# Kernel optimization log

Measured on AMD Instinct MI355X. Metric: run time of the kernel, lower is better.

The kernel has to match this reference:

```python
import jax, jax.numpy as jnp
import numpy as np

B, H, W, C = 64, 224, 224, 3
P = 16
DIM = 768
DEPTH = 12
NH, DH = 12, 64
FF = 3072
NPATCH = (H // P) * (W // P)   # 196
L = NPATCH + 1                 # 197 tokens (CLS + patches)
KEEP = int(L * (1.0 - 0.75))   # 49 unmasked tokens


def setup_inputs() -> dict:
    key = jax.random.key(0)
    ks = jax.random.split(key, 16)
    s = 0.02
    inp = {
        'inputs': jax.random.normal(ks[0], (B, H, W, C), jnp.float32),
        'conv_w': jax.random.normal(ks[1], (P, P, C, DIM), jnp.float32) * s,
        'ct':     jax.random.normal(ks[2], (1, 1, DIM), jnp.float32) * s,
        'pe':     jax.random.normal(ks[3], (1, L, DIM), jnp.float32) * s,
        'ln1_s': jnp.ones((DEPTH, DIM), jnp.float32),
        'ln1_b': jnp.zeros((DEPTH, DIM), jnp.float32),
        'qkv_w': jax.random.normal(ks[4], (DEPTH, DIM, 3 * NH * DH), jnp.float32) * s,
        'proj_w': jax.random.normal(ks[5], (DEPTH, NH * DH, DIM), jnp.float32) * s,
        'ln2_s': jnp.ones((DEPTH, DIM), jnp.float32),
        'ln2_b': jnp.zeros((DEPTH, DIM), jnp.float32),
        'w1': jax.random.normal(ks[6], (DEPTH, DIM, FF), jnp.float32) * s,
        'b1': jnp.zeros((DEPTH, FF), jnp.float32),
        'w2': jax.random.normal(ks[7], (DEPTH, FF, DIM), jnp.float32) * s,
        'b2': jnp.zeros((DEPTH, DIM), jnp.float32),
        # Faithful to original: permutation of arange(1, L+1); max value 197
        # is out-of-range and gets clamped by JAX gather, exactly as upstream.
        'mask_idx': jax.random.permutation(ks[8], jnp.arange(1, L + 1))[:KEEP].astype(jnp.int32),
    }
    return inp


def _layernorm(x, scale, bias, eps=1e-9):
    m = jnp.mean(x, axis=-1, keepdims=True)
    v = jnp.var(x, axis=-1, keepdims=True)
    return (x - m) * jax.lax.rsqrt(v + eps) * scale + bias


def _encoder(x, layer_params):
    # x: [B, KEEP, DIM]; layer_params leaves stacked on axis 0 (DEPTH)
    inv_sqrt_d = 1.0 / jnp.sqrt(jnp.float32(DH))

    def block(x, p):
        ln1s, ln1b, qw, pw, ln2s, ln2b, w1, b1, w2, b2 = p
        h = _layernorm(x, ln1s, ln1b)
        qkv = h @ qw                                   # [B, Lk, 3*NH*DH]
        q, k, v = jnp.split(qkv, 3, axis=-1)
        def heads(t):
            return t.reshape(x.shape[0], -1, NH, DH).transpose(0, 2, 1, 3)
        q, k, v = heads(q), heads(k), heads(v)         # [B, NH, Lk, DH]
        att = jax.nn.softmax(jnp.einsum('bhqd,bhkd->bhqk', q, k) * inv_sqrt_d)
        o = jnp.einsum('bhqk,bhkd->bhqd', att, v)
        o = o.transpose(0, 2, 1, 3).reshape(x.shape[0], -1, NH * DH) @ pw
        x = x + o
        h2 = _layernorm(x, ln2s, ln2b)
        x = x + (jax.nn.gelu(h2 @ w1 + b1) @ w2 + b2)
        return x, None

    x, _ = jax.lax.scan(block, x, layer_params)
    return x


def reference(inputs, conv_w, ct, pe, ln1_s, ln1_b, qkv_w, proj_w,
              ln2_s, ln2_b, w1, b1, w2, b2, mask_idx):
    # patch embed: stride-P conv, no bias
    out = jax.lax.conv_general_dilated(
        inputs, conv_w, window_strides=(P, P), padding='VALID',
        dimension_numbers=('NHWC', 'HWIO', 'NHWC'))      # [B, 14, 14, DIM]
    out = out.reshape(out.shape[0], -1, out.shape[3])     # [B, 196, DIM]
    out = jnp.concatenate((jnp.repeat(ct, out.shape[0], axis=0), out), axis=1)
    out = out + pe                                        # [B, 197, DIM]
    patches = out[:, mask_idx]                            # [B, 49, DIM]
    layer_params = (ln1_s, ln1_b, qkv_w, proj_w, ln2_s, ln2_b, w1, b1, w2, b2)
    return _encoder(patches, layer_params)
```

## Files before the change

kernel.cpp:

```cpp
#include <hip/hip_runtime.h>
#include <hip/hip_bf16.h>
#include <math.h>

#define DIMV   768
#define BATCH  64
#define KEEPT  49
#define MTOK   (BATCH*KEEPT)
#define NHEADS 12
#define DHEAD  64
#define FFV    3072
#define NDEPTH 12

typedef short short8 __attribute__((ext_vector_type(8)));
typedef float floatx4 __attribute__((ext_vector_type(4)));
typedef unsigned short ushort;
typedef unsigned short ushortx8 __attribute__((ext_vector_type(8)));

__device__ __forceinline__ ushort f2bf(float f) {
  __hip_bfloat16 h = __float2bfloat16(f);
  return *(ushort*)&h;
}

__device__ __forceinline__ void async_cp16(const void* g, void* l) {
  __builtin_amdgcn_global_load_lds((const __attribute__((address_space(1))) void*)g,
                                   (__attribute__((address_space(3))) void*)l,
                                   16, 0, 0);
}

__global__ __launch_bounds__(256) void gather_patches(
    const float* __restrict__ inp, const int* __restrict__ mask,
    __hip_bfloat16* __restrict__ apix)
{
  int gid = blockIdx.x * 256 + threadIdx.x;
  if (gid >= MTOK * DIMV) return;
  int r = gid / DIMV, k = gid - r * DIMV;
  int b = r / KEEPT, t = r - b * KEEPT;
  int j = mask[t];
  j = j < 0 ? 0 : (j > 196 ? 196 : j);
  float v = 0.f;
  if (j > 0) {
    int p  = j - 1, py = p / 14, px = p - py * 14;
    int ky = k / 48, rem = k - ky * 48, kx = rem / 3, c = rem - kx * 3;
    v = inp[(((b * 224) + py * 16 + ky) * 224 + px * 16 + kx) * 3 + c];
  }
  apix[gid] = __float2bfloat16(v);
}

__global__ __launch_bounds__(256) void layernorm_k(
    const float* __restrict__ x, const float* __restrict__ sc,
    const float* __restrict__ bi, __hip_bfloat16* __restrict__ out)
{
  __shared__ float red[8];
  int r = blockIdx.x;
  const float* xr = x + (size_t)r * DIMV;
  int t = threadIdx.x;
  float v[3];
  float s = 0.f, ss = 0.f;
#pragma unroll
  for (int i = 0; i < 3; i++) {
    float a = xr[t + i * 256];
    v[i] = a; s += a; ss += a * a;
  }
#pragma unroll
  for (int off = 32; off > 0; off >>= 1) {
    s  += __shfl_down(s,  off, 64);
    ss += __shfl_down(ss, off, 64);
  }
  int wave = t >> 6, lane = t & 63;
  if (lane == 0) { red[wave] = s; red[4 + wave] = ss; }
  __syncthreads();
  if (t == 0) {
    float a  = red[0] + red[1] + red[2] + red[3];
    float b2 = red[4] + red[5] + red[6] + red[7];
    float m  = a * (1.f / DIMV);
    float var = b2 * (1.f / DIMV) - m * m;
    red[0] = m;
    red[1] = rsqrtf(var + 1e-9f);
  }
  __syncthreads();
  float m = red[0], rs = red[1];
  __hip_bfloat16* outr = out + (size_t)r * DIMV;
#pragma unroll
  for (int i = 0; i < 3; i++) {
    int d = t + i * 256;
    outr[d] = __float2bfloat16((v[i] - m) * rs * sc[d] + bi[d]);
  }
}

__device__ __forceinline__ void transpose_tile64(
    const float* __restrict__ src, __hip_bfloat16* __restrict__ dst,
    int R, int C, int tr, int tcc)
{
  __shared__ float lds[64][65];
  const int tid = threadIdx.x;
  const int r0 = tr * 64, c0 = tcc * 64;
  const int lr = tid >> 4, lc4 = (tid & 15) * 4;
#pragma unroll
  for (int p = 0; p < 4; p++) {
    float4 v = *(const float4*)(src + (size_t)(r0 + p * 16 + lr) * C + c0 + lc4);
    lds[p * 16 + lr][lc4 + 0] = v.x;
    lds[p * 16 + lr][lc4 + 1] = v.y;
    lds[p * 16 + lr][lc4 + 2] = v.z;
    lds[p * 16 + lr][lc4 + 3] = v.w;
  }
  __syncthreads();
  const int c = tid >> 2, rc = (tid & 3) * 8;
  ushortx8 o0, o1;
#pragma unroll
  for (int j = 0; j < 8; j++) o0[j] = f2bf(lds[rc + j][c]);
#pragma unroll
  for (int j = 0; j < 8; j++) o1[j] = f2bf(lds[rc + 32 + j][c]);
  ushort* drow = (ushort*)dst + (size_t)(c0 + c) * R + r0;
  *(ushortx8*)(drow + rc)      = o0;
  *(ushortx8*)(drow + rc + 32) = o1;
}

__global__ __launch_bounds__(256) void transpose_one(
    const float* __restrict__ src, __hip_bfloat16* __restrict__ dst, int R, int C)
{
  int tc = C >> 6;
  transpose_tile64(src, dst, R, C, blockIdx.x / tc, blockIdx.x % tc);
}

#define QKV_TE  ((size_t)2304*768)
#define PROJ_TE ((size_t)768*768)
#define W1_TE   ((size_t)3072*768)
#define W2_TE   ((size_t)768*3072)
#define LSTRIDE (QKV_TE + PROJ_TE + W1_TE + W2_TE)

__global__ __launch_bounds__(256) void convert_weights(
    const float* __restrict__ qkv_w, const float* __restrict__ proj_w,
    const float* __restrict__ w1, const float* __restrict__ w2,
    __hip_bfloat16* __restrict__ dstBase, int layer0, size_t dstStride)
{
  int l = layer0 + blockIdx.y;
  __hip_bfloat16* d = dstBase + (size_t)blockIdx.y * dstStride;
  int tile = blockIdx.x;
  const float* src; __hip_bfloat16* dst; int R, C, t0;
  if (tile < 432)       { src = qkv_w  + (size_t)l*768*2304; dst = d;                          R=768;  C=2304; t0=tile; }
  else if (tile < 576)  { src = proj_w + (size_t)l*768*768;  dst = d + QKV_TE;                 R=768;  C=768;  t0=tile-432; }
  else if (tile < 1152) { src = w1     + (size_t)l*768*3072; dst = d + QKV_TE+PROJ_TE;         R=768;  C=3072; t0=tile-576; }
  else                  { src = w2     + (size_t)l*3072*768; dst = d + QKV_TE+PROJ_TE+W1_TE;   R=3072; C=768;  t0=tile-1152; }
  int tc = C >> 6;
  transpose_tile64(src, dst, R, C, t0 / tc, t0 % tc);
}

enum { EPI_NONE = 0, EPI_RESID = 1, EPI_BIAS_GELU = 2, EPI_BIAS_RESID = 3,
       EPI_EMBED = 4 };

template <int TN, int EPI, bool OUT_BF16>
__global__ __launch_bounds__(256) void gemm_mfma(
    const ushort* __restrict__ A, const ushort* __restrict__ Bt,
    const float* __restrict__ Cin, const float* __restrict__ bias,
    const float* __restrict__ pe, const int* __restrict__ mask,
    void* __restrict__ Cout, int M, int N, int K)
{
  constexpr int AM = (TN == 128) ? 4 : 2;
  constexpr int B_LOADS = TN / 64;
  __shared__ ushort As[128 * 32];
  __shared__ ushort Bs[TN * 32];

  const int tid  = threadIdx.x;
  const int wave = tid >> 6, lane = tid & 63;
  const int bm = blockIdx.y, bn = blockIdx.x;

  const int wm0 = (TN == 128) ? (wave & 1) * 64 : wave * 32;
  const int wn0 = (TN == 128) ? (wave >> 1) * 64 : 0;

  floatx4 acc[AM][4];
#pragma unroll
  for (int i = 0; i < AM; i++)
#pragma unroll
    for (int j = 0; j < 4; j++) { floatx4 z = {0.f,0.f,0.f,0.f}; acc[i][j] = z; }

  const int lrow = lane >> 2, lchunk = (lane & 3) * 8;
  const ushort* aSrc[2];
  ushort*       aDst[2];
#pragma unroll
  for (int i = 0; i < 2; i++) {
    int row = bm * 128 + (wave * 2 + i) * 16 + lrow;
    row = row < M - 1 ? row : M - 1;
    aSrc[i] = A + (size_t)row * K + lchunk;
    aDst[i] = As + (wave * 2 + i) * 512;
  }
  const ushort* bSrc[B_LOADS];
  ushort*       bDst[B_LOADS];
#pragma unroll
  for (int i = 0; i < B_LOADS; i++) {
    int row = bn * TN + (wave * B_LOADS + i) * 16 + lrow;
    bSrc[i] = Bt + (size_t)row * K + lchunk;
    bDst[i] = Bs + (wave * B_LOADS + i) * 512;
  }

  for (int k0 = 0; k0 < K; k0 += 32) {
    __syncthreads();
#pragma unroll
    for (int i = 0; i < 2; i++)       async_cp16(aSrc[i] + k0, aDst[i]);
#pragma unroll
    for (int i = 0; i < B_LOADS; i++) async_cp16(bSrc[i] + k0, bDst[i]);
    __syncthreads();

    short8 af[AM], bf[4];
#pragma unroll
    for (int mt = 0; mt < AM; mt++)
      af[mt] = *(const short8*)&As[(wm0 + mt * 16 + (lane & 15)) * 32 + (lane >> 4) * 8];
#pragma unroll
    for (int nt = 0; nt < 4; nt++)
      bf[nt] = *(const short8*)&Bs[(wn0 + nt * 16 + (lane & 15)) * 32 + (lane >> 4) * 8];
#pragma unroll
    for (int mt = 0; mt < AM; mt++)
#pragma unroll
      for (int nt = 0; nt < 4; nt++)
        acc[mt][nt] = __builtin_amdgcn_mfma_f32_16x16x32_bf16(af[mt], bf[nt], acc[mt][nt], 0, 0, 0);
  }

  const int colb = bn * TN + wn0 + (lane & 15);
  const int rq   = (lane >> 4) * 4;
#pragma unroll
  for (int mt = 0; mt < AM; mt++) {
#pragma unroll
    for (int r = 0; r < 4; r++) {
      int row = bm * 128 + wm0 + mt * 16 + rq + r;
      if (row >= M) continue;
#pragma unroll
      for (int nt = 0; nt < 4; nt++) {
        int col = colb + nt * 16;
        float u = acc[mt][nt][r];
        if (EPI == EPI_BIAS_GELU || EPI == EPI_BIAS_RESID) u += bias[col];
        if (EPI == EPI_BIAS_GELU) {
          float t3 = u * u * u;
          u = 0.5f * u * (1.f + tanhf(0.7978845608028654f * (u + 0.044715f * t3)));
        }
        if (EPI == EPI_RESID || EPI == EPI_BIAS_RESID) u += Cin[(size_t)row * N + col];
        if (EPI == EPI_EMBED) {
          int t = row % KEEPT;
          int j = mask[t];
          j = j < 0 ? 0 : (j > 196 ? 196 : j);
          if (j == 0) u = bias[col];
          u += pe[(size_t)j * DIMV + col];
        }
        if (OUT_BF16)
          ((__hip_bfloat16*)Cout)[(size_t)row * N + col] = __float2bfloat16(u);
        else
          ((float*)Cout)[(size_t)row * N + col] = u;
      }
    }
  }
}

__global__ __launch_bounds__(256) void attn_mfma(
    const ushort* __restrict__ qkv, ushort* __restrict__ o)
{
  __shared__ ushort qA[64 * 72];
  __shared__ ushort kB[64 * 72];
  __shared__ ushort vT[64 * 72];
  __shared__ ushort pA[64 * 72];
  const int b = blockIdx.x, hh = blockIdx.y;
  const int tid = threadIdx.x;
  const int wave = tid >> 6, lane = tid & 63;
  const int fr = lane & 15, fc = lane >> 4;

  const ushort* base = qkv + (size_t)b * KEEPT * (3 * DIMV) + hh * 64;

#pragma unroll
  for (int it = 0; it < 2; it++) {
    int r  = it * 32 + wave * 8 + (lane >> 3);
    int cc = (lane & 7) * 8;
    short8 qv = {0,0,0,0,0,0,0,0};
    short8 kv = {0,0,0,0,0,0,0,0};
    if (r < KEEPT) {
      const ushort* row = base + (size_t)r * (3 * DIMV);
      qv = *(const short8*)(row + cc);
      kv = *(const short8*)(row + DIMV + cc);
    }
    *(short8*)&qA[r * 72 + cc] = qv;
    *(short8*)&kB[r * 72 + cc] = kv;
  }
  for (int r = wave; r < 64; r += 4) {
    ushort v = 0;
    if (r < KEEPT) v = base[(size_t)r * (3 * DIMV) + 2 * DIMV + lane];
    vT[lane * 72 + r] = v;
  }
  __syncthreads();

  const int q0 = wave * 16;
  floatx4 sacc[4];
#pragma unroll
  for (int nt = 0; nt < 4; nt++) { floatx4 z = {0.f,0.f,0.f,0.f}; sacc[nt] = z; }

#pragma unroll
  for (int kk = 0; kk < 2; kk++) {
    const int ch = kk * 32 + fc * 8;
    short8 af = *(const short8*)&qA[(q0 + fr) * 72 + ch];
#pragma unroll
    for (int nt = 0; nt < 4; nt++) {
      short8 bf = *(const short8*)&kB[(nt * 16 + fr) * 72 + ch];
      sacc[nt] = __builtin_amdgcn_mfma_f32_16x16x32_bf16(af, bf, sacc[nt], 0, 0, 0);
    }
  }

  float inv[4];
#pragma unroll
  for (int r = 0; r < 4; r++) {
    float mx = -1e30f;
#pragma unroll
    for (int nt = 0; nt < 4; nt++) {
      float s = sacc[nt][r] * 0.125f;
      if (nt == 3 && fr >= 1) s = -1e30f;
      sacc[nt][r] = s;
      mx = fmaxf(mx, s);
    }
    mx = fmaxf(mx, __shfl_xor(mx, 1, 64));
    mx = fmaxf(mx, __shfl_xor(mx, 2, 64));
    mx = fmaxf(mx, __shfl_xor(mx, 4, 64));
    mx = fmaxf(mx, __shfl_xor(mx, 8, 64));
    float sum = 0.f;
#pragma unroll
    for (int nt = 0; nt < 4; nt++) {
      float e = __expf(sacc[nt][r] - mx);
      sacc[nt][r] = e;
      sum += e;
    }
    sum += __shfl_xor(sum, 1, 64);
    sum += __shfl_xor(sum, 2, 64);
    sum += __shfl_xor(sum, 4, 64);
    sum += __shfl_xor(sum, 8, 64);
    inv[r] = 1.f / sum;
  }

#pragma unroll
  for (int r = 0; r < 4; r++)
#pragma unroll
    for (int nt = 0; nt < 4; nt++)
      pA[(q0 + fc * 4 + r) * 72 + nt * 16 + fr] = f2bf(sacc[nt][r]);
  __syncthreads();

  floatx4 oacc[4];
#pragma unroll
  for (int nt = 0; nt < 4; nt++) { floatx4 z = {0.f,0.f,0.f,0.f}; oacc[nt] = z; }

#pragma unroll
  for (int kk = 0; kk < 2; kk++) {
    const int ch = kk * 32 + fc * 8;
    short8 af = *(const short8*)&pA[(q0 + fr) * 72 + ch];
#pragma unroll
    for (int nt = 0; nt < 4; nt++) {
      short8 bf = *(const short8*)&vT[(nt * 16 + fr) * 72 + ch];
      oacc[nt] = __builtin_amdgcn_mfma_f32_16x16x32_bf16(af, bf, oacc[nt], 0, 0, 0);
    }
  }

  ushort* obase = o + (size_t)b * KEEPT * DIMV + hh * 64;
#pragma unroll
  for (int r = 0; r < 4; r++) {
    int q = q0 + fc * 4 + r;
    if (q < KEEPT) {
#pragma unroll
      for (int nt = 0; nt < 4; nt++)
        obase[(size_t)q * DIMV + nt * 16 + fr] = f2bf(oacc[nt][r] * inv[r]);
    }
  }
}

extern "C" void kernel_launch(void* const* d_in, const int* in_sizes, int n_in,
                              void* d_out, int out_size, void* d_ws, size_t ws_size,
                              hipStream_t stream)
{
  (void)in_sizes; (void)n_in; (void)out_size;
  const float* inputs = (const float*)d_in[0];
  const float* conv_w = (const float*)d_in[1];
  const float* ct     = (const float*)d_in[2];
  const float* pe     = (const float*)d_in[3];
  const float* ln1_s  = (const float*)d_in[4];
  const float* ln1_b  = (const float*)d_in[5];
  const float* qkv_w  = (const float*)d_in[6];
  const float* proj_w = (const float*)d_in[7];
  const float* ln2_s  = (const float*)d_in[8];
  const float* ln2_b  = (const float*)d_in[9];
  const float* w1     = (const float*)d_in[10];
  const float* b1     = (const float*)d_in[11];
  const float* w2     = (const float*)d_in[12];
  const float* b2     = (const float*)d_in[13];
  const int*   mask   = (const int*)d_in[14];
  float* out = (float*)d_out;

  char* wsb = (char*)d_ws;
  float*          x     = (float*)wsb;
  __hip_bfloat16* h     = (__hip_bfloat16*)(wsb + 9633792);
  __hip_bfloat16* big   = (__hip_bfloat16*)(wsb + 9633792 + 4816896);
  __hip_bfloat16* convT = (__hip_bfloat16*)(wsb + 9633792 + 4816896 + 19267584);
  __hip_bfloat16* wbuf  = (__hip_bfloat16*)(wsb + 9633792 + 4816896 + 19267584 + 1179648);
  const size_t base_bytes = 9633792ull + 4816896 + 19267584 + 1179648;
  const bool all_mode = ws_size >= base_bytes + 12ull * LSTRIDE * 2;

  __hip_bfloat16* apix = h;
  __hip_bfloat16* qkv  = big;
  __hip_bfloat16* g    = big;

  dim3 blk(256);
  const int nelem = MTOK * DIMV;
  const int nblk  = (nelem + 255) / 256;
  const int mg    = (MTOK + 127) / 128;

  transpose_one<<<144, blk, 0, stream>>>(conv_w, convT, 768, 768);
  if (all_mode)
    convert_weights<<<dim3(1728, 12), blk, 0, stream>>>(
        qkv_w, proj_w, w1, w2, wbuf, 0, LSTRIDE);

  gather_patches<<<nblk, blk, 0, stream>>>(inputs, mask, apix);
  gemm_mfma<64, EPI_EMBED, false><<<dim3(12, mg), blk, 0, stream>>>(
      (const ushort*)apix, (const ushort*)convT, nullptr, ct, pe, mask, x,
      MTOK, DIMV, DIMV);

  for (int l = 0; l < NDEPTH; l++) {
    __hip_bfloat16* wl = wbuf + (all_mode ? (size_t)l * LSTRIDE : 0);
    if (!all_mode)
      convert_weights<<<dim3(1728, 1), blk, 0, stream>>>(
          qkv_w, proj_w, w1, w2, wbuf, l, 0);
    const ushort* qkvT  = (const ushort*)wl;
    const ushort* projT = (const ushort*)(wl + QKV_TE);
    const ushort* w1T   = (const ushort*)(wl + QKV_TE + PROJ_TE);
    const ushort* w2T   = (const ushort*)(wl + QKV_TE + PROJ_TE + W1_TE);

    layernorm_k<<<MTOK, blk, 0, stream>>>(x, ln1_s + l * DIMV, ln1_b + l * DIMV, h);
    gemm_mfma<128, EPI_NONE, true><<<dim3(18, mg), blk, 0, stream>>>(
        (const ushort*)h, qkvT, nullptr, nullptr, nullptr, nullptr, qkv,
        MTOK, 3 * DIMV, DIMV);
    attn_mfma<<<dim3(BATCH, NHEADS), blk, 0, stream>>>(
        (const ushort*)qkv, (ushort*)h);
    gemm_mfma<64, EPI_RESID, false><<<dim3(12, mg), blk, 0, stream>>>(
        (const ushort*)h, projT, x, nullptr, nullptr, nullptr, x,
        MTOK, DIMV, DIMV);
    layernorm_k<<<MTOK, blk, 0, stream>>>(x, ln2_s + l * DIMV, ln2_b + l * DIMV, h);
    gemm_mfma<128, EPI_BIAS_GELU, true><<<dim3(24, mg), blk, 0, stream>>>(
        (const ushort*)h, w1T, nullptr, b1 + (size_t)l * FFV, nullptr, nullptr, g,
        MTOK, FFV, DIMV);
    float* dst = (l == NDEPTH - 1) ? out : x;
    gemm_mfma<64, EPI_BIAS_RESID, false><<<dim3(12, mg), blk, 0, stream>>>(
        (const ushort*)g, w2T, x, b2 + (size_t)l * DIMV, nullptr, nullptr, dst,
        MTOK, DIMV, FFV);
  }
}
```

Measured before the change: 2.495 ms.

## Double-buffer GEMM LDS tiles with BK=64, XOR swizzle, and unified 128x64 tiling

The MFMA GEMM now uses double-buffered LDS tiles with a K-step of 64. The next tile's async global-to-LDS copy is issued before the current tile's MFMAs, so there is one barrier per iteration instead of two. LDS columns are XOR-swizzled to reduce bank conflicts, and MFMA sections get raised wave priority. All GEMMs now use a single 128x64 tile shape, which doubles the grid for the QKV and FC1 GEMMs and raises LDS use per block, possibly lowering occupancy.

```diff
diff --git a/kernel.cpp b/kernel.cpp
--- a/kernel.cpp
+++ b/kernel.cpp
@@ -148,79 +148,109 @@
 enum { EPI_NONE = 0, EPI_RESID = 1, EPI_BIAS_GELU = 2, EPI_BIAS_RESID = 3,
        EPI_EMBED = 4 };
 
-template <int TN, int EPI, bool OUT_BF16>
+template <int EPI, bool OUT_BF16>
 __global__ __launch_bounds__(256) void gemm_mfma(
     const ushort* __restrict__ A, const ushort* __restrict__ Bt,
     const float* __restrict__ Cin, const float* __restrict__ bias,
     const float* __restrict__ pe, const int* __restrict__ mask,
     void* __restrict__ Cout, int M, int N, int K)
 {
-  constexpr int AM = (TN == 128) ? 4 : 2;
-  constexpr int B_LOADS = TN / 64;
-  __shared__ ushort As[128 * 32];
-  __shared__ ushort Bs[TN * 32];
+  __shared__ ushort As[2][128 * 64];
+  __shared__ ushort Bs[2][64 * 64];
 
   const int tid  = threadIdx.x;
   const int wave = tid >> 6, lane = tid & 63;
   const int bm = blockIdx.y, bn = blockIdx.x;
-
-  const int wm0 = (TN == 128) ? (wave & 1) * 64 : wave * 32;
-  const int wn0 = (TN == 128) ? (wave >> 1) * 64 : 0;
-
-  floatx4 acc[AM][4];
-#pragma unroll
-  for (int i = 0; i < AM; i++)
+  const int fr = lane & 15, fc = lane >> 4;
+
+  floatx4 acc[2][4];
+#pragma unroll
+  for (int i = 0; i < 2; i++)
 #pragma unroll
     for (int j = 0; j < 4; j++) { floatx4 z = {0.f,0.f,0.f,0.f}; acc[i][j] = z; }
 
-  const int lrow = lane >> 2, lchunk = (lane & 3) * 8;
-  const ushort* aSrc[2];
-  ushort*       aDst[2];
-#pragma unroll
-  for (int i = 0; i < 2; i++) {
-    int row = bm * 128 + (wave * 2 + i) * 16 + lrow;
+  const int lrow   = lane >> 3;
+  const int lchunk = ((lane & 7) ^ lrow) * 8;
+  const ushort* aSrc[4];
+#pragma unroll
+  for (int i = 0; i < 4; i++) {
+    int row = bm * 128 + wave * 32 + i * 8 + lrow;
     row = row < M - 1 ? row : M - 1;
     aSrc[i] = A + (size_t)row * K + lchunk;
-    aDst[i] = As + (wave * 2 + i) * 512;
-  }
-  const ushort* bSrc[B_LOADS];
-  ushort*       bDst[B_LOADS];
-#pragma unroll
-  for (int i = 0; i < B_LOADS; i++) {
-    int row = bn * TN + (wave * B_LOADS + i) * 16 + lrow;
+  }
+  const ushort* bSrc[2];
+#pragma unroll
+  for (int i = 0; i < 2; i++) {
+    int row = bn * 64 + wave * 16 + i * 8 + lrow;
     bSrc[i] = Bt + (size_t)row * K + lchunk;
-    bDst[i] = Bs + (wave * B_LOADS + i) * 512;
-  }
-
-  for (int k0 = 0; k0 < K; k0 += 32) {
-    __syncthreads();
-#pragma unroll
-    for (int i = 0; i < 2; i++)       async_cp16(aSrc[i] + k0, aDst[i]);
-#pragma unroll
-    for (int i = 0; i < B_LOADS; i++) async_cp16(bSrc[i] + k0, bDst[i]);
-    __syncthreads();
-
-    short8 af[AM], bf[4];
-#pragma unroll
-    for (int mt = 0; mt < AM; mt++)
-      af[mt] = *(const short8*)&As[(wm0 + mt * 16 + (lane & 15)) * 32 + (lane >> 4) * 8];
-#pragma unroll
-    for (int nt = 0; nt < 4; nt++)
-      bf[nt] = *(const short8*)&Bs[(wn0 + nt * 16 + (lane & 15)) * 32 + (lane >> 4) * 8];
-#pragma unroll
-    for (int mt = 0; mt < AM; mt++)
+  }
+
+  const int NT = K >> 6;
+
+  {
+    ushort* aD = &As[0][(wave * 32) * 64];
+#pragma unroll
+    for (int i = 0; i < 4; i++) async_cp16(aSrc[i], aD + i * 8 * 64);
+    ushort* bD = &Bs[0][(wave * 16) * 64];
+#pragma unroll
+    for (int i = 0; i < 2; i++) async_cp16(bSrc[i], bD + i * 8 * 64);
+  }
+  asm volatile("s_waitcnt vmcnt(0)" ::: "memory");
+  __builtin_amdgcn_s_barrier();
+  __builtin_amdgcn_sched_barrier(0);
+
+  int cur = 0;
+  for (int t = 0; t < NT; t++) {
+    if (t + 1 < NT) {
+      const int k0 = (t + 1) << 6;
+      ushort* aD = &As[cur ^ 1][(wave * 32) * 64];
+#pragma unroll
+      for (int i = 0; i < 4; i++) async_cp16(aSrc[i] + k0, aD + i * 8 * 64);
+      ushort* bD = &Bs[cur ^ 1][(wave * 16) * 64];
+#pragma unroll
+      for (int i = 0; i < 2; i++) async_cp16(bSrc[i] + k0, bD + i * 8 * 64);
+    }
+
+    const ushort* Ab = As[cur];
+    const ushort* Bb = Bs[cur];
+    short8 af[2][2], bf[2][4];
+#pragma unroll
+    for (int kk = 0; kk < 2; kk++) {
+      const int cbase = kk * 4 + fc;
+      const int slot  = (cbase ^ (fr & 7)) * 8;
+#pragma unroll
+      for (int mt = 0; mt < 2; mt++)
+        af[kk][mt] = *(const short8*)&Ab[(wave * 32 + mt * 16 + fr) * 64 + slot];
 #pragma unroll
       for (int nt = 0; nt < 4; nt++)
-        acc[mt][nt] = __builtin_amdgcn_mfma_f32_16x16x32_bf16(af[mt], bf[nt], acc[mt][nt], 0, 0, 0);
-  }
-
-  const int colb = bn * TN + wn0 + (lane & 15);
-  const int rq   = (lane >> 4) * 4;
-#pragma unroll
-  for (int mt = 0; mt < AM; mt++) {
+        bf[kk][nt] = *(const short8*)&Bb[(nt * 16 + fr) * 64 + slot];
+    }
+    __builtin_amdgcn_s_setprio(1);
+#pragma unroll
+    for (int kk = 0; kk < 2; kk++)
+#pragma unroll
+      for (int mt = 0; mt < 2; mt++)
+#pragma unroll
+        for (int nt = 0; nt < 4; nt++)
+          acc[mt][nt] = __builtin_amdgcn_mfma_f32_16x16x32_bf16(
+              af[kk][mt], bf[kk][nt], acc[mt][nt], 0, 0, 0);
+    __builtin_amdgcn_s_setprio(0);
+
+    if (t + 1 < NT) {
+      asm volatile("s_waitcnt vmcnt(0)" ::: "memory");
+      __builtin_amdgcn_s_barrier();
+      __builtin_amdgcn_sched_barrier(0);
+    }
+    cur ^= 1;
+  }
+
+  const int colb = bn * 64 + fr;
+  const int rq   = fc * 4;
+#pragma unroll
+  for (int mt = 0; mt < 2; mt++) {
 #pragma unroll
     for (int r = 0; r < 4; r++) {
-      int row = bm * 128 + wm0 + mt * 16 + rq + r;
+      int row = bm * 128 + wave * 32 + mt * 16 + rq + r;
       if (row >= M) continue;
 #pragma unroll
       for (int nt = 0; nt < 4; nt++) {
@@ -408,7 +438,7 @@
         qkv_w, proj_w, w1, w2, wbuf, 0, LSTRIDE);
 
   gather_patches<<<nblk, blk, 0, stream>>>(inputs, mask, apix);
-  gemm_mfma<64, EPI_EMBED, false><<<dim3(12, mg), blk, 0, stream>>>(
+  gemm_mfma<EPI_EMBED, false><<<dim3(12, mg), blk, 0, stream>>>(
       (const ushort*)apix, (const ushort*)convT, nullptr, ct, pe, mask, x,
       MTOK, DIMV, DIMV);
 
@@ -423,20 +453,20 @@
     const ushort* w2T   = (const ushort*)(wl + QKV_TE + PROJ_TE + W1_TE);
 
     layernorm_k<<<MTOK, blk, 0, stream>>>(x, ln1_s + l * DIMV, ln1_b + l * DIMV, h);
-    gemm_mfma<128, EPI_NONE, true><<<dim3(18, mg), blk, 0, stream>>>(
+    gemm_mfma<EPI_NONE, true><<<dim3(36, mg), blk, 0, stream>>>(
         (const ushort*)h, qkvT, nullptr, nullptr, nullptr, nullptr, qkv,
         MTOK, 3 * DIMV, DIMV);
     attn_mfma<<<dim3(BATCH, NHEADS), blk, 0, stream>>>(
         (const ushort*)qkv, (ushort*)h);
-    gemm_mfma<64, EPI_RESID, false><<<dim3(12, mg), blk, 0, stream>>>(
+    gemm_mfma<EPI_RESID, false><<<dim3(12, mg), blk, 0, stream>>>(
         (const ushort*)h, projT, x, nullptr, nullptr, nullptr, x,
         MTOK, DIMV, DIMV);
     layernorm_k<<<MTOK, blk, 0, stream>>>(x, ln2_s + l * DIMV, ln2_b + l * DIMV, h);
-    gemm_mfma<128, EPI_BIAS_GELU, true><<<dim3(24, mg), blk, 0, stream>>>(
+    gemm_mfma<EPI_BIAS_GELU, true><<<dim3(48, mg), blk, 0, stream>>>(
         (const ushort*)h, w1T, nullptr, b1 + (size_t)l * FFV, nullptr, nullptr, g,
         MTOK, FFV, DIMV);
     float* dst = (l == NDEPTH - 1) ? out : x;
-    gemm_mfma<64, EPI_BIAS_RESID, false><<<dim3(12, mg), blk, 0, stream>>>(
+    gemm_mfma<EPI_BIAS_RESID, false><<<dim3(12, mg), blk, 0, stream>>>(
         (const ushort*)g, w2T, x, b2 + (size_t)l * DIMV, nullptr, nullptr, dst,
         MTOK, DIMV, FFV);
   }
```

Result: faster. 2.297 ms (-7.9%).
